# Kernel tuning notes

Hardware: AMD Instinct MI355X
Metric: run time of the kernel (lower is better)

## Reference

```python
import math
import jax, jax.numpy as jnp
import numpy as np

B, L0, IN, D, H, FF, PRED = 16, 4096, 8, 256, 8, 1024, 24
NLAYERS = 3
FACTOR = 5

def _u(L):
    return max(1, min(FACTOR * math.ceil(math.log(L + 1)), L))

def _ln(x, g, b, eps=1e-5):
    m = x.mean(-1, keepdims=True)
    v = ((x - m) ** 2).mean(-1, keepdims=True)
    return (x - m) * jax.lax.rsqrt(v + eps) * g + b

def _prob_attn(h, idx, wq, bq, wk, bk, wv, bv, wo, bo):
    B_, L, Dm = h.shape
    dk = Dm // H
    scale = 1.0 / math.sqrt(dk)
    def proj(w, b):
        return (h @ w + b).reshape(B_, L, H, dk).transpose(0, 2, 1, 3)
    Q, K, V = proj(wq, bq), proj(wk, bk), proj(wv, bv)  # [B,H,L,dk]
    u = idx.shape[0]
    Ks = K[:, :, idx, :]                                   # sampled keys [B,H,u,dk]
    scores = jnp.einsum('bhld,bhud->bhlu', Q, Ks) * scale
    M = scores.max(-1) - scores.mean(-1)                   # sparsity score [B,H,L]
    top = jax.lax.top_k(M, u)[1]                           # top-u queries [B,H,u]
    Qt = jnp.take_along_axis(Q, top[..., None], axis=2)    # [B,H,u,dk]
    attn = jax.nn.softmax(jnp.einsum('bhud,bhld->bhul', Qt, K) * scale, axis=-1)
    ctx_top = jnp.einsum('bhul,bhld->bhud', attn, V)       # [B,H,u,dk]
    ctx = jnp.broadcast_to(V.mean(2, keepdims=True), (B_, H, L, dk))
    bh = B_ * H
    ctx = ctx.reshape(bh, L, dk).at[jnp.arange(bh)[:, None], top.reshape(bh, u)].set(ctx_top.reshape(bh, u, dk))
    ctx = ctx.reshape(B_, H, L, dk).transpose(0, 2, 1, 3).reshape(B_, L, Dm)
    return ctx @ wo + bo

def _distill(x, w, b):
    # Conv1d(k=3,pad=1) + ELU + MaxPool1d(2)
    xc = x.transpose(0, 2, 1)  # [B,D,L]
    y = jax.lax.conv_general_dilated(xc, w, (1,), [(1, 1)], dimension_numbers=('NCH', 'OIH', 'NCH')) + b[None, :, None]
    y = jax.nn.elu(y)
    y = jax.lax.reduce_window(y, -jnp.inf, jax.lax.max, (1, 1, 2), (1, 1, 2), 'VALID')
    return y.transpose(0, 2, 1)

def _forward(x, in_w, in_b, pos_emb, qw, qb, kw, kb, vw, vb, ow, ob, f1w, f1b, f2w, f2b, n1g, n1b, n2g, n2b, cw, cb, fcw, fcb, idxs):
    Bx, L, _ = x.shape
    h = x @ in_w + in_b + pos_emb[None, :L]
    for i in range(NLAYERS):
        a = _prob_attn(h, idxs[i], qw[i], qb[i], kw[i], kb[i], vw[i], vb[i], ow[i], ob[i])
        h = _ln(h + a, n1g[i], n1b[i])
        f = jax.nn.gelu(h @ f1w[i] + f1b[i], approximate=False) @ f2w[i] + f2b[i]
        h = _ln(h + f, n2g[i], n2b[i])
        if i < NLAYERS - 1:
            h = _distill(h, cw[i], cb[i])
    return h[:, -1, :] @ fcw + fcb

def setup_inputs():
    key = jax.random.key(0)
    ks = jax.random.split(key, 16)
    s = 0.02
    d = {}
    d['x'] = jax.random.normal(ks[0], (B, L0, IN), jnp.float32)
    Ls = [L0, L0 // 2, L0 // 4]
    for i, Li in enumerate(Ls):
        d[f'idx{i}'] = jax.random.randint(ks[1 + i], (_u(Li),), 0, Li, jnp.int32)
    d['in_w'] = jax.random.normal(ks[4], (IN, D)) * s
    d['in_b'] = jnp.zeros((D,))
    d['pos_emb'] = jax.random.normal(ks[5], (L0, D)) * s
    d['qw'] = jax.random.normal(ks[6], (NLAYERS, D, D)) * s
    d['qb'] = jnp.zeros((NLAYERS, D))
    d['kw'] = jax.random.normal(ks[7], (NLAYERS, D, D)) * s
    d['kb'] = jnp.zeros((NLAYERS, D))
    d['vw'] = jax.random.normal(ks[8], (NLAYERS, D, D)) * s
    d['vb'] = jnp.zeros((NLAYERS, D))
    d['ow'] = jax.random.normal(ks[9], (NLAYERS, D, D)) * s
    d['ob'] = jnp.zeros((NLAYERS, D))
    d['f1w'] = jax.random.normal(ks[10], (NLAYERS, D, FF)) * s
    d['f1b'] = jnp.zeros((NLAYERS, FF))
    d['f2w'] = jax.random.normal(ks[11], (NLAYERS, FF, D)) * s
    d['f2b'] = jnp.zeros((NLAYERS, D))
    d['n1g'] = jnp.ones((NLAYERS, D))
    d['n1b'] = jnp.zeros((NLAYERS, D))
    d['n2g'] = jnp.ones((NLAYERS, D))
    d['n2b'] = jnp.zeros((NLAYERS, D))
    d['cw'] = jax.random.normal(ks[12], (NLAYERS - 1, D, D, 3)) * s
    d['cb'] = jnp.zeros((NLAYERS - 1, D))
    d['fcw'] = jax.random.normal(ks[13], (D, PRED)) * s
    d['fcb'] = jnp.zeros((PRED,))
    return d

def reference(x, idx0, idx1, idx2, in_w, in_b, pos_emb, qw, qb, kw, kb, vw, vb, ow, ob, f1w, f1b, f2w, f2b, n1g, n1b, n2g, n2b, cw, cb, fcw, fcb):
    return _forward(x, in_w, in_b, pos_emb, qw, qb, kw, kb, vw, vb, ow, ob, f1w, f1b, f2w, f2b, n1g, n1b, n2g, n2b, cw, cb, fcw, fcb, (idx0, idx1, idx2))
```

## Files before the change

### kernel.cpp

```cpp
#include <hip/hip_runtime.h>
#include <hip/hip_bf16.h>
#include <math.h>

typedef __hip_bfloat16 bf16;
typedef __attribute__((ext_vector_type(8))) short short8;
typedef __attribute__((ext_vector_type(4))) float floatx4;

#define B_    16
#define L0_   4096
#define IN_   8
#define D_    256
#define H_    8
#define DK_   32
#define FF_   1024
#define PRED_ 24
#define UMAX_ 48
#define NS_   4
#define NSV_  8
#define SCALE_ 0.17677669529663687f

__device__ __forceinline__ float b2f(bf16 v) { return __bfloat162float(v); }
__device__ __forceinline__ bf16  f2b(float v){ return __float2bfloat16(v); }
__device__ __forceinline__ float gelu_exact(float x){
  return 0.5f * x * (1.0f + erff(x * 0.7071067811865476f));
}
__device__ __forceinline__ float eluf(float x){ return x > 0.f ? x : (expf(x) - 1.f); }
__device__ __forceinline__ float ldf(const void* p, size_t i, int f){
  return f ? ((const float*)p)[i] : b2f(((const bf16*)p)[i]);
}
__device__ __forceinline__ void gld16(const void* g, const short* l){
  __builtin_amdgcn_global_load_lds(
      (const __attribute__((address_space(1))) unsigned int*)g,
      (__attribute__((address_space(3))) unsigned int*)l, 16, 0, 0);
}
__device__ __forceinline__ void unpack8(uint4 v, float* o){
  o[0] = __uint_as_float(v.x << 16); o[1] = __uint_as_float(v.x & 0xffff0000u);
  o[2] = __uint_as_float(v.y << 16); o[3] = __uint_as_float(v.y & 0xffff0000u);
  o[4] = __uint_as_float(v.z << 16); o[5] = __uint_as_float(v.z & 0xffff0000u);
  o[6] = __uint_as_float(v.w << 16); o[7] = __uint_as_float(v.w & 0xffff0000u);
}
__device__ __forceinline__ void unpack4(uint2 v, float* o){
  o[0] = __uint_as_float(v.x << 16); o[1] = __uint_as_float(v.x & 0xffff0000u);
  o[2] = __uint_as_float(v.y << 16); o[3] = __uint_as_float(v.y & 0xffff0000u);
}
__device__ __forceinline__ unsigned pack2(float a, float b){
  bf16 x = f2b(a), y = f2b(b);
  return (unsigned)*(unsigned short*)&x | ((unsigned)*(unsigned short*)&y << 16);
}
__device__ __forceinline__ void ld_row32(const bf16* p, float* o){
  const uint4* q = (const uint4*)p;
  uint4 a = q[0], b = q[1], c = q[2], d = q[3];
  unpack8(a, o); unpack8(b, o + 8); unpack8(c, o + 16); unpack8(d, o + 24);
}

__global__ __launch_bounds__(256) void detect_mode_kernel(
    const unsigned short* __restrict__ x16, int* __restrict__ flag,
    bf16* __restrict__ zbuf)
{
  int tid = threadIdx.x;
  if (tid < 32) zbuf[tid] = f2b(0.f);
  int cnt = 0;
  for (int i = tid; i < 512; i += 256) {
    unsigned short v = x16[2 * i];
    int expo = (v >> 7) & 0xFF;
    if (expo >= 0x90) cnt++;
  }
  __shared__ int red[256];
  red[tid] = cnt;
  __syncthreads();
  for (int s = 128; s > 0; s >>= 1) {
    if (tid < s) red[tid] += red[tid + s];
    __syncthreads();
  }
  if (tid == 0) flag[0] = (red[0] > 8) ? 1 : 0;
}

__global__ __launch_bounds__(256) void canon_kernel(
    const void* __restrict__ src, bf16* __restrict__ dst, int n,
    const int* __restrict__ flag)
{
  int i = blockIdx.x * 256 + threadIdx.x;
  if (i >= n) return;
  dst[i] = f2b(ldf(src, i, flag[0]));
}

__global__ __launch_bounds__(256) void transpose_w_kernel(
    const void* __restrict__ src, bf16* __restrict__ dst, int K, int N,
    const int* __restrict__ flag, int lstride)
{
  int i = blockIdx.x * 256 + threadIdx.x;
  if (i >= K * N) return;
  size_t soff = (size_t)blockIdx.y * K * N;
  int k = i / N, n = i % N;
  dst[(size_t)blockIdx.y * lstride + (size_t)n * K + k] = f2b(ldf(src, soff + i, flag[0]));
}

__global__ __launch_bounds__(256) void transpose_cw_kernel(
    const void* __restrict__ src, bf16* __restrict__ dst,
    const int* __restrict__ flag)
{
  int i = blockIdx.x * 256 + threadIdx.x;
  if (i >= D_ * D_ * 3) return;
  size_t off = (size_t)blockIdx.y * D_ * D_ * 3;
  int o = i / (D_ * 3), c = (i / 3) % D_, t = i % 3;
  dst[off + ((size_t)t * D_ + o) * D_ + c] = f2b(ldf(src, off + i, flag[0]));
}

__global__ __launch_bounds__(256) void embed_kernel(
    const void* __restrict__ x, const void* __restrict__ in_w,
    const void* __restrict__ in_b, const void* __restrict__ pos,
    const int* __restrict__ flag, bf16* __restrict__ h)
{
  int d = threadIdx.x;
  int f = flag[0];
  float wcol[IN_];
#pragma unroll
  for (int k = 0; k < IN_; ++k) wcol[k] = ldf(in_w, k * D_ + d, f);
  float bd = ldf(in_b, d, f);
  int t0 = blockIdx.x * 8;
#pragma unroll
  for (int t = 0; t < 8; ++t) {
    int token = t0 + t;
    int l = token & (L0_ - 1);
    float s = bd + ldf(pos, (size_t)l * D_ + d, f);
#pragma unroll
    for (int k = 0; k < IN_; ++k)
      s += ldf(x, (size_t)token * IN_ + k, f) * wcol[k];
    h[(size_t)token * D_ + d] = f2b(s);
  }
}

template<int ACT, int HM>
__global__ __launch_bounds__(256) void mfma_gemm(
    const bf16* __restrict__ A, const bf16* __restrict__ Wt,
    const bf16* __restrict__ b0, const bf16* __restrict__ b1,
    const bf16* __restrict__ b2, bf16* __restrict__ C,
    int M, int N, int K, int Lsh, size_t partStride, int cn)
{
  __shared__ short As[128 * 64];
  __shared__ short Bs[128 * 64];
  int tid = threadIdx.x;
  int w = tid >> 6, lane = tid & 63;
  int ln = lane & 15, qd = lane >> 4;
  int id = blockIdx.x;
  int idx = id >> 3;
  int cblk = idx % cn;
  int rblk = (id & 7) + ((idx / cn) << 3);
  int bm = rblk << 7, bn = cblk << 7;
  int wm = (w >> 1) << 6, wn = (w & 1) << 6;

  floatx4 acc[4][4];
#pragma unroll
  for (int mi = 0; mi < 4; ++mi)
#pragma unroll
    for (int ni = 0; ni < 4; ++ni) {
      acc[mi][ni][0] = 0.f; acc[mi][ni][1] = 0.f;
      acc[mi][ni][2] = 0.f; acc[mi][ni][3] = 0.f;
    }

  int rr[4], ofs[4];
#pragma unroll
  for (int t = 0; t < 4; ++t) {
    int p = (w << 8) + (t << 6) + lane;
    int r = p >> 3;
    ofs[t] = (((p & 7) ^ (r & 7)) << 3);
    rr[t] = r;
  }
  const bf16* pA[4]; const bf16* pB[4]; short* dst[4];
#pragma unroll
  for (int t = 0; t < 4; ++t) {
    pA[t] = A + (size_t)(bm + rr[t]) * K + ofs[t];
    pB[t] = Wt + (size_t)(bn + rr[t]) * K + ofs[t];
    dst[t] = As + (((w << 2) + t) << 9);
  }

  for (int k0 = 0; k0 < K; k0 += 64) {
    __syncthreads();
#pragma unroll
    for (int t = 0; t < 4; ++t) gld16(pA[t] + k0, dst[t]);
#pragma unroll
    for (int t = 0; t < 4; ++t) gld16(pB[t] + k0, dst[t] + 128 * 64);
    __syncthreads();
#pragma unroll
    for (int kb = 0; kb < 2; ++kb) {
      short8 af[4], bff[4];
#pragma unroll
      for (int mi = 0; mi < 4; ++mi) {
        int r = wm + mi * 16 + ln;
        af[mi] = *(const short8*)(As + (r << 6) + ((((kb << 2) + qd) ^ (r & 7)) << 3));
      }
#pragma unroll
      for (int ni = 0; ni < 4; ++ni) {
        int r = wn + ni * 16 + ln;
        bff[ni] = *(const short8*)(Bs + (r << 6) + ((((kb << 2) + qd) ^ (r & 7)) << 3));
      }
#pragma unroll
      for (int mi = 0; mi < 4; ++mi)
#pragma unroll
        for (int ni = 0; ni < 4; ++ni)
          acc[mi][ni] = __builtin_amdgcn_mfma_f32_16x16x32_bf16(
              af[mi], bff[ni], acc[mi][ni], 0, 0, 0);
    }
  }

#pragma unroll
  for (int ni = 0; ni < 4; ++ni) {
    int col = bn + wn + ni * 16 + ln;
    const bf16* bsel = b0;
    int cm = col;
    if (HM) {
      int part = col >> 8;
      cm = col & 255;
      bsel = (part == 0) ? b0 : ((part == 1) ? b1 : b2);
    }
    float bv = b2f(bsel[cm]);
    int part = HM ? (col >> 8) : 0;
    int hh = cm >> 5, dk = cm & 31;
#pragma unroll
    for (int mi = 0; mi < 4; ++mi) {
      int row = bm + wm + mi * 16 + (qd << 2);
#pragma unroll
      for (int r = 0; r < 4; ++r) {
        float v = acc[mi][ni][r] + bv;
        if (ACT == 1) v = gelu_exact(v);
        if (HM) {
          int rr2 = row + r;
          int bb = rr2 >> Lsh, ll = rr2 & ((1 << Lsh) - 1);
          C[part * partStride + ((((size_t)(bb * H_ + hh)) << Lsh) + ll) * 32 + dk] = f2b(v);
        } else {
          C[(size_t)(row + r) * N + col] = f2b(v);
        }
      }
    }
  }
}

__global__ __launch_bounds__(256) void mfma_conv_distill(
    const bf16* __restrict__ hsrc, const bf16* __restrict__ WtC,
    const bf16* __restrict__ cb, bf16* __restrict__ outp,
    const bf16* __restrict__ zbuf, int L)
{
  __shared__ short As[128 * 32];
  __shared__ short Bs[128 * 32];
  int tid = threadIdx.x;
  int w = tid >> 6, lane = tid & 63;
  int ln = lane & 15, qd = lane >> 4;
  int id = blockIdx.x;
  int idx = id >> 3;
  int cblk = idx & 1;
  int rblk = (id & 7) + ((idx >> 1) << 3);
  int bn = cblk << 7;
  int bpb = L >> 7;
  int b = rblk / bpb;
  int p0 = (rblk % bpb) << 7;
  int wm = (w >> 1) << 6, wn = (w & 1) << 6;

  floatx4 acc[4][4];
#pragma unroll
  for (int mi = 0; mi < 4; ++mi)
#pragma unroll
    for (int ni = 0; ni < 4; ++ni) {
      acc[mi][ni][0] = 0.f; acc[mi][ni][1] = 0.f;
      acc[mi][ni][2] = 0.f; acc[mi][ni][3] = 0.f;
    }

  int s0 = (w << 7) + lane, s1 = s0 + 64;
  int r0 = s0 >> 2, c0 = (s0 & 3) ^ (r0 & 3);
  int r1 = s1 >> 2, c1 = (s1 & 3) ^ (r1 & 3);
  short* ldsA = As + (w << 10);
  short* ldsB = Bs + (w << 10);

  for (int tap = 0; tap < 3; ++tap) {
    const bf16* wt = WtC + (size_t)tap * D_ * D_;
    int pos0 = p0 + r0 + tap - 1;
    int pos1 = p0 + r1 + tap - 1;
    const bf16* gA0 = (pos0 >= 0 && pos0 < L)
        ? hsrc + ((size_t)b * L + pos0) * D_ + (c0 << 3) : zbuf;
    const bf16* gA1 = (pos1 >= 0 && pos1 < L)
        ? hsrc + ((size_t)b * L + pos1) * D_ + (c1 << 3) : zbuf;
    int stepA0 = (pos0 >= 0 && pos0 < L) ? 1 : 0;
    int stepA1 = (pos1 >= 0 && pos1 < L) ? 1 : 0;
    const bf16* gB0 = wt + (size_t)(bn + r0) * D_ + (c0 << 3);
    const bf16* gB1 = wt + (size_t)(bn + r1) * D_ + (c1 << 3);
    for (int k0 = 0; k0 < D_; k0 += 32) {
      __syncthreads();
      gld16(gA0 + (size_t)k0 * stepA0, ldsA);
      gld16(gA1 + (size_t)k0 * stepA1, ldsA + 512);
      gld16(gB0 + k0, ldsB);
      gld16(gB1 + k0, ldsB + 512);
      __syncthreads();
      short8 af[4], bff[4];
#pragma unroll
      for (int mi = 0; mi < 4; ++mi) {
        int r = wm + mi * 16 + ln;
        af[mi] = *(const short8*)(As + (r << 5) + ((qd ^ (r & 3)) << 3));
      }
#pragma unroll
      for (int ni = 0; ni < 4; ++ni) {
        int r = wn + ni * 16 + ln;
        bff[ni] = *(const short8*)(Bs + (r << 5) + ((qd ^ (r & 3)) << 3));
      }
#pragma unroll
      for (int mi = 0; mi < 4; ++mi)
#pragma unroll
        for (int ni = 0; ni < 4; ++ni)
          acc[mi][ni] = __builtin_amdgcn_mfma_f32_16x16x32_bf16(
              af[mi], bff[ni], acc[mi][ni], 0, 0, 0);
    }
  }

  int Lh = L >> 1;
#pragma unroll
  for (int ni = 0; ni < 4; ++ni) {
    int col = bn + wn + ni * 16 + ln;
    float bv = b2f(cb[col]);
#pragma unroll
    for (int mi = 0; mi < 4; ++mi) {
      float y0 = eluf(acc[mi][ni][0] + bv);
      float y1 = eluf(acc[mi][ni][1] + bv);
      float y2 = eluf(acc[mi][ni][2] + bv);
      float y3 = eluf(acc[mi][ni][3] + bv);
      int prow = (p0 + wm + mi * 16 + (qd << 2)) >> 1;
      outp[((size_t)b * Lh + prow) * D_ + col]     = f2b(fmaxf(y0, y1));
      outp[((size_t)b * Lh + prow + 1) * D_ + col] = f2b(fmaxf(y2, y3));
    }
  }
}

__global__ __launch_bounds__(256) void prob_scores_kernel(
    const bf16* __restrict__ Qh, const bf16* __restrict__ Kh,
    const int* __restrict__ idx, float* __restrict__ Mout, int L, int u)
{
  __shared__ float ks[UMAX_][32];
  int tid = threadIdx.x;
  int bpb = L >> 8;
  int bh = blockIdx.x / bpb;
  int l  = (blockIdx.x % bpb) * 256 + tid;
  if (tid < u * 4) {
    int t = tid >> 2, c = tid & 3;
    int ls = idx[t];
    if (ls < 0) ls = 0; if (ls >= L) ls = L - 1;
    uint4 v = *(const uint4*)(Kh + ((size_t)bh * L + ls) * 32 + c * 8);
    unpack8(v, &ks[t][c * 8]);
  }
  __syncthreads();
  float qv[32];
  ld_row32(Qh + ((size_t)bh * L + l) * 32, qv);
  float mx = -3.4e38f, sm = 0.f;
  for (int t = 0; t < u; ++t) {
    float s = 0.f;
#pragma unroll
    for (int j4 = 0; j4 < 8; ++j4) {
      float4 k4 = *(const float4*)&ks[t][j4 * 4];
      s += qv[4*j4+0]*k4.x + qv[4*j4+1]*k4.y + qv[4*j4+2]*k4.z + qv[4*j4+3]*k4.w;
    }
    s *= SCALE_;
    mx = fmaxf(mx, s);
    sm += s;
  }
  Mout[(size_t)bh * L + l] = mx - sm / (float)u;
}

__global__ __launch_bounds__(256) void topk_kernel(
    const float* __restrict__ M, int* __restrict__ top, int L, int u)
{
  __shared__ unsigned int hist[256];
  __shared__ unsigned int prefS, kS;
  __shared__ int cntG, tieCnt;
  __shared__ int tieList[256];
  int bh = blockIdx.x;
  int tid = threadIdx.x;
  int w = tid >> 6, lane = tid & 63;
  int nper = L >> 8;

  unsigned int key[16];
  for (int i = 0; i < nper; ++i) {
    unsigned int ub = __float_as_uint(M[(size_t)bh * L + i * 256 + tid]);
    key[i] = (ub & 0x80000000u) ? ~ub : (ub | 0x80000000u);
  }

  unsigned int pref = 0, k = (unsigned int)u;
  for (int round = 0; round < 4; ++round) {
    int shift = 24 - (round << 3);
    hist[tid] = 0;
    __syncthreads();
    for (int i = 0; i < nper; ++i) {
      unsigned int kk = key[i];
      if (round == 0 || (kk >> (shift + 8)) == pref)
        atomicAdd(&hist[(kk >> shift) & 0xFFu], 1u);
    }
    __syncthreads();
    if (w == 0) {
      int d0 = lane << 2;
      unsigned int h0 = hist[d0], h1 = hist[d0 + 1];
      unsigned int h2 = hist[d0 + 2], h3 = hist[d0 + 3];
      unsigned int lsum = h0 + h1 + h2 + h3;
      unsigned int incl = lsum;
#pragma unroll
      for (int off = 1; off < 64; off <<= 1) {
        unsigned int o = __shfl_down(incl, off);
        if (lane + off < 64) incl += o;
      }
      unsigned int e3 = incl - lsum;
      unsigned int e2 = e3 + h3;
      unsigned int e1 = e2 + h2;
      unsigned int e0 = e1 + h1;
      if (e3 < k && k <= e3 + h3) { prefS = (pref << 8) | (d0 + 3); kS = k - e3; }
      if (e2 < k && k <= e2 + h2) { prefS = (pref << 8) | (d0 + 2); kS = k - e2; }
      if (e1 < k && k <= e1 + h1) { prefS = (pref << 8) | (d0 + 1); kS = k - e1; }
      if (e0 < k && k <= e0 + h0) { prefS = (pref << 8) | (d0 + 0); kS = k - e0; }
    }
    __syncthreads();
    pref = prefS;
    k = kS;
    __syncthreads();
  }

  unsigned int T = pref;
  if (tid == 0) { cntG = 0; tieCnt = 0; }
  __syncthreads();
  for (int i = 0; i < nper; ++i) {
    unsigned int kk = key[i];
    int lidx = i * 256 + tid;
    if (kk > T) {
      int pos = atomicAdd(&cntG, 1);
      if (pos < u) top[bh * u + pos] = lidx;
    } else if (kk == T) {
      int tpos = atomicAdd(&tieCnt, 1);
      if (tpos < 256) tieList[tpos] = lidx;
    }
  }
  __syncthreads();
  if (tid == 0) {
    int base = cntG;
    int E = tieCnt; if (E > 256) E = 256;
    for (int t = 0; t < (int)k && base + t < u; ++t) {
      int best = 0x7fffffff, bj = -1;
      for (int j = 0; j < E; ++j) {
        int v = tieList[j];
        if (v >= 0 && v < best) { best = v; bj = j; }
      }
      if (bj >= 0) { tieList[bj] = -1; top[bh * u + base + t] = best; }
      else top[bh * u + base + t] = 0;
    }
  }
}

__global__ __launch_bounds__(256) void topq_attn_mfma(
    const bf16* __restrict__ Qh, const bf16* __restrict__ Kh,
    const bf16* __restrict__ Vh, const int* __restrict__ top,
    float* __restrict__ part_m, float* __restrict__ part_s,
    float* __restrict__ part_acc, int L, int u)
{
  __shared__ short Qs[64 * 32];
  __shared__ short Ks[128 * 32];
  __shared__ short Vs[128 * 32];
  __shared__ short Ps[4][64 * 32];
  __shared__ float mrow[64];
  __shared__ float redm[4][64];
  __shared__ float redl[4][64];

  int bh = blockIdx.x, sl = blockIdx.y;
  int tid = threadIdx.x;
  int w = tid >> 6, lane = tid & 63;
  int ln = lane & 15, qd = lane >> 4;
  int Ls = L / NS_;
  int lbase = sl * Ls;
  const bf16* Kbase = Kh + (size_t)bh * L * 32;
  const bf16* Vbase = Vh + (size_t)bh * L * 32;

  {
    int r = tid >> 2, cpos = tid & 3, corig = cpos ^ (r & 3);
    uint4 v = make_uint4(0, 0, 0, 0);
    if (r < u) {
      int lq = top[bh * u + r];
      if (lq < 0) lq = 0; if (lq >= L) lq = L - 1;
      v = *(const uint4*)(Qh + ((size_t)bh * L + lq) * 32 + corig * 8);
    }
    *(uint4*)(Qs + r * 32 + cpos * 8) = v;
  }
  __syncthreads();

  short8 aq[4];
#pragma unroll
  for (int mi = 0; mi < 4; ++mi) {
    int r = mi * 16 + ln;
    aq[mi] = *(const short8*)(Qs + (r << 5) + ((qd ^ (r & 3)) << 3));
  }

  int s0 = (w << 7) + lane, s1 = s0 + 64;
  int r0 = s0 >> 2, c0 = (s0 & 3) ^ (r0 & 3);
  int r1 = s1 >> 2, c1 = (s1 & 3) ^ (r1 & 3);
  short* ldsK = Ks + (w << 10);
  short* ldsV = Vs + (w << 10);
  int nch = Ls >> 7;

  float m_run[16];
#pragma unroll
  for (int i = 0; i < 16; ++i) m_run[i] = -3.4e38f;

  for (int ch = 0; ch < nch; ++ch) {
    int tok0 = lbase + (ch << 7);
    __syncthreads();
    gld16(Kbase + (size_t)(tok0 + r0) * 32 + (c0 << 3), ldsK);
    gld16(Kbase + (size_t)(tok0 + r1) * 32 + (c1 << 3), ldsK + 512);
    __syncthreads();
    short8 bk[2];
#pragma unroll
    for (int ni = 0; ni < 2; ++ni) {
      int r = (w << 5) + ni * 16 + ln;
      bk[ni] = *(const short8*)(Ks + (r << 5) + ((qd ^ (r & 3)) << 3));
    }
#pragma unroll
    for (int mi = 0; mi < 4; ++mi)
#pragma unroll
      for (int ni = 0; ni < 2; ++ni) {
        floatx4 s = {0.f, 0.f, 0.f, 0.f};
        s = __builtin_amdgcn_mfma_f32_16x16x32_bf16(aq[mi], bk[ni], s, 0, 0, 0);
#pragma unroll
        for (int r = 0; r < 4; ++r)
          m_run[mi * 4 + r] = fmaxf(m_run[mi * 4 + r], s[r] * SCALE_);
      }
  }
#pragma unroll
  for (int i = 0; i < 16; ++i) {
    float v = m_run[i];
    v = fmaxf(v, __shfl_xor(v, 1));
    v = fmaxf(v, __shfl_xor(v, 2));
    v = fmaxf(v, __shfl_xor(v, 4));
    v = fmaxf(v, __shfl_xor(v, 8));
    m_run[i] = v;
  }
  if (ln == 0) {
#pragma unroll
    for (int mi = 0; mi < 4; ++mi)
#pragma unroll
      for (int r = 0; r < 4; ++r)
        redm[w][mi * 16 + qd * 4 + r] = m_run[mi * 4 + r];
  }
  __syncthreads();
  if (tid < 64)
    mrow[tid] = fmaxf(fmaxf(redm[0][tid], redm[1][tid]),
                      fmaxf(redm[2][tid], redm[3][tid]));
  __syncthreads();

  float l_run[16];
#pragma unroll
  for (int i = 0; i < 16; ++i) l_run[i] = 0.f;
  floatx4 oacc[4][2];
#pragma unroll
  for (int mi = 0; mi < 4; ++mi)
#pragma unroll
    for (int ni = 0; ni < 2; ++ni) {
      oacc[mi][ni][0] = 0.f; oacc[mi][ni][1] = 0.f;
      oacc[mi][ni][2] = 0.f; oacc[mi][ni][3] = 0.f;
    }
  bf16* myPs = (bf16*)Ps[w];

  for (int ch = 0; ch < nch; ++ch) {
    int tok0 = lbase + (ch << 7);
    __syncthreads();
    gld16(Kbase + (size_t)(tok0 + r0) * 32 + (c0 << 3), ldsK);
    gld16(Kbase + (size_t)(tok0 + r1) * 32 + (c1 << 3), ldsK + 512);
    gld16(Vbase + (size_t)(tok0 + r0) * 32 + (c0 << 3), ldsV);
    gld16(Vbase + (size_t)(tok0 + r1) * 32 + (c1 << 3), ldsV + 512);
    __syncthreads();
    short8 bk[2];
#pragma unroll
    for (int ni = 0; ni < 2; ++ni) {
      int r = (w << 5) + ni * 16 + ln;
      bk[ni] = *(const short8*)(Ks + (r << 5) + ((qd ^ (r & 3)) << 3));
    }
#pragma unroll
    for (int mi = 0; mi < 4; ++mi)
#pragma unroll
      for (int ni = 0; ni < 2; ++ni) {
        floatx4 s = {0.f, 0.f, 0.f, 0.f};
        s = __builtin_amdgcn_mfma_f32_16x16x32_bf16(aq[mi], bk[ni], s, 0, 0, 0);
#pragma unroll
        for (int r = 0; r < 4; ++r) {
          int row = mi * 16 + qd * 4 + r;
          float p = expf(s[r] * SCALE_ - mrow[row]);
          l_run[mi * 4 + r] += p;
          int tl = ni * 16 + ln;
          myPs[(row << 5) + (((tl >> 3) ^ (row & 3)) << 3) + (tl & 7)] = f2b(p);
        }
      }
    __syncthreads();
    short8 ap[4];
#pragma unroll
    for (int mi = 0; mi < 4; ++mi) {
      int r = mi * 16 + ln;
      ap[mi] = *(const short8*)((short*)myPs + (r << 5) + ((qd ^ (r & 3)) << 3));
    }
    short8 bv[2];
#pragma unroll
    for (int ni = 0; ni < 2; ++ni) {
      short tmp[8];
#pragma unroll
      for (int j = 0; j < 8; ++j) {
        int tok = (w << 5) + (qd << 3) + j;
        int dk = ni * 16 + ln;
        tmp[j] = Vs[(tok << 5) + (((dk >> 3) ^ (tok & 3)) << 3) + (dk & 7)];
      }
      bv[ni] = *(short8*)tmp;
    }
#pragma unroll
    for (int mi = 0; mi < 4; ++mi)
#pragma unroll
      for (int ni = 0; ni < 2; ++ni)
        oacc[mi][ni] = __builtin_amdgcn_mfma_f32_16x16x32_bf16(
            ap[mi], bv[ni], oacc[mi][ni], 0, 0, 0);
  }

#pragma unroll
  for (int i = 0; i < 16; ++i) {
    float v = l_run[i];
    v += __shfl_xor(v, 1); v += __shfl_xor(v, 2);
    v += __shfl_xor(v, 4); v += __shfl_xor(v, 8);
    l_run[i] = v;
  }
  if (ln == 0) {
#pragma unroll
    for (int mi = 0; mi < 4; ++mi)
#pragma unroll
      for (int r = 0; r < 4; ++r)
        redl[w][mi * 16 + qd * 4 + r] = l_run[mi * 4 + r];
  }
  __syncthreads();

  size_t pb = (size_t)sl * (B_ * H_) + bh;
  if (tid < UMAX_) {
    part_m[pb * UMAX_ + tid] = mrow[tid];
    part_s[pb * UMAX_ + tid] =
        redl[0][tid] + redl[1][tid] + redl[2][tid] + redl[3][tid];
  }
#pragma unroll
  for (int mi = 0; mi < 4; ++mi) {
#pragma unroll
    for (int ni = 0; ni < 2; ++ni) {
#pragma unroll
      for (int r = 0; r < 4; ++r) {
        int row = mi * 16 + qd * 4 + r;
        if (row < UMAX_) {
          int dk = ni * 16 + ln;
          part_acc[((pb * UMAX_ + row) << 7) + (w << 5) + dk] = oacc[mi][ni][r];
        }
      }
    }
  }
}

__global__ __launch_bounds__(256) void attn_combine_kernel(
    const float* __restrict__ part_m, const float* __restrict__ part_s,
    const float* __restrict__ part_acc, float* __restrict__ ctx_top, int u)
{
  int bh = blockIdx.x;
  for (int i = threadIdx.x; i < u * 32; i += 256) {
    int q = i >> 5, dk = i & 31;
    float M = -3.4e38f;
#pragma unroll
    for (int s = 0; s < NS_; ++s)
      M = fmaxf(M, part_m[((size_t)s * (B_ * H_) + bh) * UMAX_ + q]);
    float num = 0.f, den = 0.f;
#pragma unroll
    for (int s = 0; s < NS_; ++s) {
      size_t pb = (size_t)s * (B_ * H_) + bh;
      float e = expf(part_m[pb * UMAX_ + q] - M);
      float a = 0.f;
#pragma unroll
      for (int w = 0; w < 4; ++w)
        a += part_acc[((pb * UMAX_ + q) << 7) + (w << 5) + dk];
      num += a * e;
      den += part_s[pb * UMAX_ + q] * e;
    }
    ctx_top[((size_t)bh * u + q) * 32 + dk] = num / den;
  }
}

__global__ __launch_bounds__(256) void vmean_part_kernel(
    const bf16* __restrict__ Vh, float* __restrict__ vpart, int L)
{
  int blk = blockIdx.x;
  int bh = blk / NSV_, s = blk % NSV_;
  int tid = threadIdx.x;
  int dk = tid & 31, lg = tid >> 5;
  int Ls = L / NSV_;
  int l0 = s * Ls;
  float acc = 0.f;
  for (int l = lg; l < Ls; l += 8)
    acc += b2f(Vh[((size_t)bh * L + l0 + l) * 32 + dk]);
  __shared__ float red[256];
  red[tid] = acc;
  __syncthreads();
  for (int st = 128; st >= 32; st >>= 1) {
    if (tid < st) red[tid] += red[tid + st];
    __syncthreads();
  }
  if (tid < 32) vpart[(size_t)blk * 32 + tid] = red[tid];
}

__global__ __launch_bounds__(32) void vmean_comb_kernel(
    const float* __restrict__ vpart, float* __restrict__ vmean, int L)
{
  int bh = blockIdx.x;
  int dk = threadIdx.x;
  float s = 0.f;
#pragma unroll
  for (int i = 0; i < NSV_; ++i)
    s += vpart[((size_t)bh * NSV_ + i) * 32 + dk];
  vmean[bh * 32 + dk] = s / (float)L;
}

__global__ __launch_bounds__(256) void fill_ctx_kernel(
    const float* __restrict__ vmean, bf16* __restrict__ ctx, int Lsh)
{
  int d = threadIdx.x;
  size_t t0 = (size_t)blockIdx.x * 8;
  int hh = d >> 5, dk = d & 31;
#pragma unroll
  for (int t = 0; t < 8; ++t) {
    size_t token = t0 + t;
    int b = (int)(token >> Lsh);
    ctx[token * D_ + d] = f2b(vmean[(b * H_ + hh) * 32 + dk]);
  }
}

__global__ __launch_bounds__(256) void scatter_kernel(
    const float* __restrict__ ctx_top, const int* __restrict__ top,
    bf16* __restrict__ ctx, int L, int u)
{
  int t = blockIdx.x * 256 + threadIdx.x;
  int total = B_ * H_ * u * DK_;
  if (t >= total) return;
  int j  = t % DK_;
  int uu = (t / DK_) % u;
  int hh = (t / (DK_ * u)) % H_;
  int b  = t / (DK_ * u * H_);
  int lq = top[(b * H_ + hh) * u + uu];
  if (lq < 0) lq = 0; if (lq >= L) lq = L - 1;
  ctx[((size_t)b * L + lq) * D_ + hh * DK_ + j] =
      f2b(ctx_top[(size_t)((b * H_ + hh) * u + uu) * DK_ + j]);
}

__global__ __launch_bounds__(256) void add_ln_kernel(
    bf16* __restrict__ h, const bf16* __restrict__ r,
    const bf16* __restrict__ g, const bf16* __restrict__ be)
{
  int w = threadIdx.x >> 6, lane = threadIdx.x & 63;
  size_t row = (size_t)blockIdx.x * 4 + w;
  bf16* hp = h + row * D_;
  const bf16* rp = r + row * D_;
  float hv[4], rv[4];
  unpack4(*(const uint2*)(hp + lane * 4), hv);
  unpack4(*(const uint2*)(rp + lane * 4), rv);
  float v0 = hv[0] + rv[0], v1 = hv[1] + rv[1];
  float v2 = hv[2] + rv[2], v3 = hv[3] + rv[3];
  float s = v0 + v1 + v2 + v3;
#pragma unroll
  for (int off = 1; off < 64; off <<= 1) s += __shfl_xor(s, off);
  float mean = s * (1.f / D_);
  float d0 = v0 - mean, d1 = v1 - mean, d2 = v2 - mean, d3 = v3 - mean;
  float q = d0 * d0 + d1 * d1 + d2 * d2 + d3 * d3;
#pragma unroll
  for (int off = 1; off < 64; off <<= 1) q += __shfl_xor(q, off);
  float rstd = rsqrtf(q * (1.f / D_) + 1e-5f);
  float gv[4], bv[4];
  unpack4(*(const uint2*)(g + lane * 4), gv);
  unpack4(*(const uint2*)(be + lane * 4), bv);
  uint2 o;
  o.x = pack2(d0 * rstd * gv[0] + bv[0], d1 * rstd * gv[1] + bv[1]);
  o.y = pack2(d2 * rstd * gv[2] + bv[2], d3 * rstd * gv[3] + bv[3]);
  *(uint2*)(hp + lane * 4) = o;
}

__global__ __launch_bounds__(256) void copy_bf16_kernel(
    bf16* __restrict__ dst, const bf16* __restrict__ src, size_t n)
{
  size_t i = (size_t)blockIdx.x * 256 + threadIdx.x;
  if (i < n) dst[i] = src[i];
}

__global__ __launch_bounds__(64) void final_fc_kernel(
    const bf16* __restrict__ h, const bf16* __restrict__ fcw,
    const bf16* __restrict__ fcb, void* __restrict__ out, int L,
    const int* __restrict__ flag)
{
  int b = blockIdx.x;
  int p = threadIdx.x;
  if (p >= PRED_) return;
  const bf16* hr = h + ((size_t)b * L + (L - 1)) * D_;
  float s = b2f(fcb[p]);
  for (int d = 0; d < D_; ++d) s += b2f(hr[d]) * b2f(fcw[d * PRED_ + p]);
  if (flag[0]) ((float*)out)[b * PRED_ + p] = s;
  else         ((bf16*)out)[b * PRED_ + p]  = f2b(s);
}

extern "C" void kernel_launch(void* const* d_in, const int* in_sizes, int n_in,
                              void* d_out, int out_size, void* d_ws, size_t ws_size,
                              hipStream_t stream)
{
  const size_t hsz = (size_t)B_ * L0_ * D_;
  char* wsc = (char*)d_ws;
  bf16* h  = (bf16*)wsc;
  bf16* Qh = (bf16*)(wsc + hsz * 2);
  bf16* Kh = (bf16*)(wsc + hsz * 4);
  bf16* Vh = (bf16*)(wsc + hsz * 6);
  char* misc = wsc + hsz * 8;
  float* Mbuf    = (float*)misc;
  float* ctx_top = Mbuf + (size_t)B_ * H_ * L0_;
  float* vmean   = ctx_top + (size_t)B_ * H_ * UMAX_ * DK_;
  int*   topbuf  = (int*)(vmean + B_ * H_ * DK_);
  int*   flag    = topbuf + B_ * H_ * UMAX_;
  float* part_m  = (float*)(flag + 4);
  float* part_s  = part_m + (size_t)NS_ * B_ * H_ * UMAX_;
  float* part_acc= part_s + (size_t)NS_ * B_ * H_ * UMAX_;
  float* vpart   = part_acc + (size_t)NS_ * B_ * H_ * UMAX_ * 128;
  bf16*  zbuf    = (bf16*)(vpart + (size_t)B_ * H_ * NSV_ * 32);
  bf16*  canon   = zbuf + 32;

  bf16* qkvT = canon;
  bf16* owT  = qkvT + 3 * 196608;
  bf16* f1wT = owT  + 3 * 65536;
  bf16* f2wT = f1wT + 3 * 262144;
  bf16* cwT  = f2wT + 3 * 262144;
  bf16* smallc = cwT + 2 * 196608;

  bf16* ctxb = Vh;
  bf16* ab   = Qh;
  bf16* t1   = Kh;
  bf16* hnext = Kh;

  detect_mode_kernel<<<1, 256, 0, stream>>>((const unsigned short*)d_in[0], flag, zbuf);

  const int cidx[13] = {8, 10, 12, 14, 16, 18, 19, 20, 21, 22, 24, 25, 26};
  bf16* cptr[27] = {};
  {
    bf16* p = smallc;
    for (int t = 0; t < 13; ++t) {
      int i = cidx[t];
      int n = in_sizes[i];
      cptr[i] = p;
      canon_kernel<<<(n + 255) / 256, 256, 0, stream>>>(d_in[i], p, n, flag);
      p += (n + 7) & ~7;
    }
  }
  transpose_w_kernel<<<dim3(256, 3), 256, 0, stream>>>(d_in[7],  qkvT,          256, 256, flag, 196608);
  transpose_w_kernel<<<dim3(256, 3), 256, 0, stream>>>(d_in[9],  qkvT + 65536,  256, 256, flag, 196608);
  transpose_w_kernel<<<dim3(256, 3), 256, 0, stream>>>(d_in[11], qkvT + 131072, 256, 256, flag, 196608);
  transpose_w_kernel<<<dim3(256, 3), 256, 0, stream>>>(d_in[13], owT,  256, 256, flag, 65536);
  transpose_w_kernel<<<dim3(1024, 3), 256, 0, stream>>>(d_in[15], f1wT, 256, 1024, flag, 262144);
  transpose_w_kernel<<<dim3(1024, 3), 256, 0, stream>>>(d_in[17], f2wT, 1024, 256, flag, 262144);
  transpose_cw_kernel<<<dim3(768, 2), 256, 0, stream>>>(d_in[23], cwT, flag);

  const int* idx[3] = {(const int*)d_in[1], (const int*)d_in[2], (const int*)d_in[3]};
  int us[3] = {in_sizes[1], in_sizes[2], in_sizes[3]};

  embed_kernel<<<B_ * L0_ / 8, 256, 0, stream>>>(d_in[0], d_in[4], d_in[5], d_in[6], flag, h);

  int L = L0_;
  for (int i = 0; i < 3; ++i) {
    int tokens = B_ * L;
    int u = us[i];
    int Lsh = 31 - __builtin_clz(L);
    int rm = tokens / 128;
    mfma_gemm<0,1><<<6 * rm, 256, 0, stream>>>(
        h, qkvT + (size_t)i * 196608,
        cptr[8] + i * D_, cptr[10] + i * D_, cptr[12] + i * D_,
        Qh, tokens, 768, 256, Lsh, hsz, 6);

    prob_scores_kernel<<<B_ * H_ * (L / 256), 256, 0, stream>>>(Qh, Kh, idx[i], Mbuf, L, u);
    topk_kernel<<<B_ * H_, 256, 0, stream>>>(Mbuf, topbuf, L, u);
    topq_attn_mfma<<<dim3(B_ * H_, NS_), 256, 0, stream>>>(
        Qh, Kh, Vh, topbuf, part_m, part_s, part_acc, L, u);
    attn_combine_kernel<<<B_ * H_, 256, 0, stream>>>(part_m, part_s, part_acc, ctx_top, u);
    vmean_part_kernel<<<B_ * H_ * NSV_, 256, 0, stream>>>(Vh, vpart, L);
    vmean_comb_kernel<<<B_ * H_, 32, 0, stream>>>(vpart, vmean, L);
    fill_ctx_kernel<<<tokens / 8, 256, 0, stream>>>(vmean, ctxb, Lsh);
    scatter_kernel<<<(B_ * H_ * u * DK_ + 255) / 256, 256, 0, stream>>>(ctx_top, topbuf, ctxb, L, u);
    mfma_gemm<0,0><<<2 * rm, 256, 0, stream>>>(
        ctxb, owT + (size_t)i * 65536, cptr[14] + i * D_, nullptr, nullptr,
        ab, tokens, 256, 256, 0, 0, 2);

    add_ln_kernel<<<tokens / 4, 256, 0, stream>>>(h, ab, cptr[19] + i * D_, cptr[20] + i * D_);

    const int CH = 16384;
    for (int c0 = 0; c0 < tokens; c0 += CH) {
      int cm = (tokens - c0 < CH) ? (tokens - c0) : CH;
      int rmc = cm / 128;
      mfma_gemm<1,0><<<8 * rmc, 256, 0, stream>>>(
          h + (size_t)c0 * D_, f1wT + (size_t)i * 262144, cptr[16] + i * FF_,
          nullptr, nullptr, t1, cm, FF_, 256, 0, 0, 8);
      mfma_gemm<0,0><<<2 * rmc, 256, 0, stream>>>(
          t1, f2wT + (size_t)i * 262144, cptr[18] + i * D_, nullptr, nullptr,
          ab + (size_t)c0 * D_, cm, 256, FF_, 0, 0, 2);
    }
    add_ln_kernel<<<tokens / 4, 256, 0, stream>>>(h, ab, cptr[21] + i * D_, cptr[22] + i * D_);

    if (i < 2) {
      int Lh = L / 2;
      mfma_conv_distill<<<2 * (B_ * (L / 128)), 256, 0, stream>>>(
          h, cwT + (size_t)i * 196608, cptr[24] + i * D_, hnext, zbuf, L);
      size_t n = (size_t)B_ * Lh * D_;
      copy_bf16_kernel<<<(unsigned)((n + 255) / 256), 256, 0, stream>>>(h, hnext, n);
      L = Lh;
    }
  }
  final_fc_kernel<<<B_, 64, 0, stream>>>(h, cptr[25], cptr[26], d_out, L, flag);
}
```

Baseline: 1.165 ms.

## Stage GEMM epilogue through LDS for vector stores; fuse ctx fill and scatter

The GEMM epilogue now writes the bf16 results into swizzled shared memory, then stores them to global memory as 16-byte vectors, in both the plain and the head-split QKV layouts. Before, each thread wrote one 2-byte value at a time. The vmean combine step is folded into fill_ctx, and attn_combine now scatters its results straight into the ctx buffer, which removes two kernels and the float ctx_top round trip. The layer copy now moves uint4 vectors. The epilogue pays for an extra LDS pass and two barriers.

```diff
diff --git a/kernel.cpp b/kernel.cpp
--- a/kernel.cpp
+++ b/kernel.cpp
@@ -21,6 +21,7 @@
 
 __device__ __forceinline__ float b2f(bf16 v) { return __bfloat162float(v); }
 __device__ __forceinline__ bf16  f2b(float v){ return __float2bfloat16(v); }
+__device__ __forceinline__ short f2s(float v){ bf16 x = f2b(v); return *(short*)&x; }
 __device__ __forceinline__ float gelu_exact(float x){
   return 0.5f * x * (1.0f + erff(x * 0.7071067811865476f));
 }
@@ -137,8 +138,9 @@
     const bf16* __restrict__ b2, bf16* __restrict__ C,
     int M, int N, int K, int Lsh, size_t partStride, int cn)
 {
-  __shared__ short As[128 * 64];
-  __shared__ short Bs[128 * 64];
+  __shared__ short smem[2 * 128 * 64];
+  short* As = smem;
+  short* Bs = smem + 128 * 64;
   int tid = threadIdx.x;
   int w = tid >> 6, lane = tid & 63;
   int ln = lane & 15, qd = lane >> 4;
@@ -203,6 +205,7 @@
     }
   }
 
+  __syncthreads();
 #pragma unroll
   for (int ni = 0; ni < 4; ++ni) {
     int col = bn + wn + ni * 16 + ln;
@@ -214,23 +217,36 @@
       bsel = (part == 0) ? b0 : ((part == 1) ? b1 : b2);
     }
     float bv = b2f(bsel[cm]);
-    int part = HM ? (col >> 8) : 0;
-    int hh = cm >> 5, dk = cm & 31;
+    int cl = wn + ni * 16 + ln;
 #pragma unroll
     for (int mi = 0; mi < 4; ++mi) {
-      int row = bm + wm + mi * 16 + (qd << 2);
+      int rowl = wm + mi * 16 + (qd << 2);
 #pragma unroll
       for (int r = 0; r < 4; ++r) {
         float v = acc[mi][ni][r] + bv;
         if (ACT == 1) v = gelu_exact(v);
-        if (HM) {
-          int rr2 = row + r;
-          int bb = rr2 >> Lsh, ll = rr2 & ((1 << Lsh) - 1);
-          C[part * partStride + ((((size_t)(bb * H_ + hh)) << Lsh) + ll) * 32 + dk] = f2b(v);
-        } else {
-          C[(size_t)(row + r) * N + col] = f2b(v);
-        }
-      }
+        int rl = rowl + r;
+        smem[(rl << 7) + ((((cl >> 3) ^ (rl & 15))) << 3) + (cl & 7)] = f2s(v);
+      }
+    }
+  }
+  __syncthreads();
+#pragma unroll
+  for (int it = 0; it < 8; ++it) {
+    int idx2 = it * 256 + tid;
+    int rl = idx2 >> 4, c = idx2 & 15;
+    uint4 v = *(const uint4*)(smem + (rl << 7) + ((c ^ (rl & 15)) << 3));
+    int row = bm + rl;
+    int colbase = bn + (c << 3);
+    if (HM) {
+      int part = colbase >> 8;
+      int cmb = colbase & 255;
+      int hh = cmb >> 5, dk = cmb & 31;
+      int bb = row >> Lsh, ll = row & ((1 << Lsh) - 1);
+      *(uint4*)(C + part * partStride +
+                ((((size_t)(bb * H_ + hh)) << Lsh) + ll) * 32 + dk) = v;
+    } else {
+      *(uint4*)(C + (size_t)row * N + colbase) = v;
     }
   }
 }
@@ -653,9 +669,11 @@
 
 __global__ __launch_bounds__(256) void attn_combine_kernel(
     const float* __restrict__ part_m, const float* __restrict__ part_s,
-    const float* __restrict__ part_acc, float* __restrict__ ctx_top, int u)
+    const float* __restrict__ part_acc, const int* __restrict__ top,
+    bf16* __restrict__ ctx, int L, int u)
 {
   int bh = blockIdx.x;
+  int b = bh >> 3, hh = bh & 7;
   for (int i = threadIdx.x; i < u * 32; i += 256) {
     int q = i >> 5, dk = i & 31;
     float M = -3.4e38f;
@@ -674,7 +692,9 @@
       num += a * e;
       den += part_s[pb * UMAX_ + q] * e;
     }
-    ctx_top[((size_t)bh * u + q) * 32 + dk] = num / den;
+    int lq = top[bh * u + q];
+    if (lq < 0) lq = 0; if (lq >= L) lq = L - 1;
+    ctx[((size_t)b * L + lq) * D_ + hh * DK_ + dk] = f2b(num / den);
   }
 }
 
@@ -700,47 +720,22 @@
   if (tid < 32) vpart[(size_t)blk * 32 + tid] = red[tid];
 }
 
-__global__ __launch_bounds__(32) void vmean_comb_kernel(
-    const float* __restrict__ vpart, float* __restrict__ vmean, int L)
-{
-  int bh = blockIdx.x;
-  int dk = threadIdx.x;
+__global__ __launch_bounds__(256) void fill_ctx_kernel(
+    const float* __restrict__ vpart, bf16* __restrict__ ctx, int Lsh, int L)
+{
+  int d = threadIdx.x;
+  size_t t0 = (size_t)blockIdx.x * 8;
+  int b = (int)(t0 >> Lsh);
+  int hh = d >> 5, dk = d & 31;
+  int bh = b * H_ + hh;
   float s = 0.f;
 #pragma unroll
   for (int i = 0; i < NSV_; ++i)
     s += vpart[((size_t)bh * NSV_ + i) * 32 + dk];
-  vmean[bh * 32 + dk] = s / (float)L;
-}
-
-__global__ __launch_bounds__(256) void fill_ctx_kernel(
-    const float* __restrict__ vmean, bf16* __restrict__ ctx, int Lsh)
-{
-  int d = threadIdx.x;
-  size_t t0 = (size_t)blockIdx.x * 8;
-  int hh = d >> 5, dk = d & 31;
-#pragma unroll
-  for (int t = 0; t < 8; ++t) {
-    size_t token = t0 + t;
-    int b = (int)(token >> Lsh);
-    ctx[token * D_ + d] = f2b(vmean[(b * H_ + hh) * 32 + dk]);
-  }
-}
-
-__global__ __launch_bounds__(256) void scatter_kernel(
-    const float* __restrict__ ctx_top, const int* __restrict__ top,
-    bf16* __restrict__ ctx, int L, int u)
-{
-  int t = blockIdx.x * 256 + threadIdx.x;
-  int total = B_ * H_ * u * DK_;
-  if (t >= total) return;
-  int j  = t % DK_;
-  int uu = (t / DK_) % u;
-  int hh = (t / (DK_ * u)) % H_;
-  int b  = t / (DK_ * u * H_);
-  int lq = top[(b * H_ + hh) * u + uu];
-  if (lq < 0) lq = 0; if (lq >= L) lq = L - 1;
-  ctx[((size_t)b * L + lq) * D_ + hh * DK_ + j] =
-      f2b(ctx_top[(size_t)((b * H_ + hh) * u + uu) * DK_ + j]);
+  bf16 v = f2b(s / (float)L);
+#pragma unroll
+  for (int t = 0; t < 8; ++t)
+    ctx[(t0 + t) * D_ + d] = v;
 }
 
 __global__ __launch_bounds__(256) void add_ln_kernel(
@@ -774,11 +769,11 @@
   *(uint2*)(hp + lane * 4) = o;
 }
 
-__global__ __launch_bounds__(256) void copy_bf16_kernel(
-    bf16* __restrict__ dst, const bf16* __restrict__ src, size_t n)
+__global__ __launch_bounds__(256) void copy16_kernel(
+    uint4* __restrict__ dst, const uint4* __restrict__ src, size_t n16)
 {
   size_t i = (size_t)blockIdx.x * 256 + threadIdx.x;
-  if (i < n) dst[i] = src[i];
+  if (i < n16) dst[i] = src[i];
 }
 
 __global__ __launch_bounds__(64) void final_fc_kernel(
@@ -873,11 +868,10 @@
     topk_kernel<<<B_ * H_, 256, 0, stream>>>(Mbuf, topbuf, L, u);
     topq_attn_mfma<<<dim3(B_ * H_, NS_), 256, 0, stream>>>(
         Qh, Kh, Vh, topbuf, part_m, part_s, part_acc, L, u);
-    attn_combine_kernel<<<B_ * H_, 256, 0, stream>>>(part_m, part_s, part_acc, ctx_top, u);
     vmean_part_kernel<<<B_ * H_ * NSV_, 256, 0, stream>>>(Vh, vpart, L);
-    vmean_comb_kernel<<<B_ * H_, 32, 0, stream>>>(vpart, vmean, L);
-    fill_ctx_kernel<<<tokens / 8, 256, 0, stream>>>(vmean, ctxb, Lsh);
-    scatter_kernel<<<(B_ * H_ * u * DK_ + 255) / 256, 256, 0, stream>>>(ctx_top, topbuf, ctxb, L, u);
+    fill_ctx_kernel<<<tokens / 8, 256, 0, stream>>>(vpart, ctxb, Lsh, L);
+    attn_combine_kernel<<<B_ * H_, 256, 0, stream>>>(
+        part_m, part_s, part_acc, topbuf, ctxb, L, u);
     mfma_gemm<0,0><<<2 * rm, 256, 0, stream>>>(
         ctxb, owT + (size_t)i * 65536, cptr[14] + i * D_, nullptr, nullptr,
         ab, tokens, 256, 256, 0, 0, 2);
@@ -901,8 +895,9 @@
       int Lh = L / 2;
       mfma_conv_distill<<<2 * (B_ * (L / 128)), 256, 0, stream>>>(
           h, cwT + (size_t)i * 196608, cptr[24] + i * D_, hnext, zbuf, L);
-      size_t n = (size_t)B_ * Lh * D_;
-      copy_bf16_kernel<<<(unsigned)((n + 255) / 256), 256, 0, stream>>>(h, hnext, n);
+      size_t n16 = (size_t)B_ * Lh * D_ / 8;
+      copy16_kernel<<<(unsigned)((n16 + 255) / 256), 256, 0, stream>>>(
+          (uint4*)h, (const uint4*)hnext, n16);
       L = Lh;
     }
   }
```

Result: slower. 1.264 ms (+8.5%).
